# Optimization experiments

Measured on AMD Instinct MI355X. Metric: run time of the kernel, lower is better.

## Reference

```python
import jax, jax.numpy as jnp
import numpy as np

# Static hypernetwork layer sizes from HyperOption(z_dim=256, inner_h=64, a_dim=32, layers=3)
SIZES = [256 * 64, 64, 64 * 64, 64, 64 * 32, 32]  # sum = 22688
SPLITS = np.cumsum(SIZES)[:-1]


def setup_inputs() -> dict:
    key = jax.random.key(0)
    ks = jax.random.split(key, 8)
    B, Z, H = 4096, 256, 1024
    return {
        "inputs": jax.random.normal(ks[0], (B, Z), dtype=jnp.float32),
        "option": jax.random.normal(ks[1], (B, sum(SIZES)), dtype=jnp.float32) * 0.05,
        "w1": jax.random.normal(ks[2], (H, Z), dtype=jnp.float32) * 0.05,
        "b1": jax.random.normal(ks[3], (H,), dtype=jnp.float32) * 0.05,
        "w2": jax.random.normal(ks[4], (H, H), dtype=jnp.float32) * 0.05,
        "b2": jax.random.normal(ks[5], (H,), dtype=jnp.float32) * 0.05,
        "w3": jax.random.normal(ks[6], (1, H), dtype=jnp.float32) * 0.05,
        "b3": jax.random.normal(ks[7], (1,), dtype=jnp.float32) * 0.05,
    }


def _apply_option(state, option):
    # Per-sample hypernetwork MLP: weights/biases packed in `option`.
    parts = jnp.split(option, SPLITS, axis=-1)
    cur = state
    n_layers = len(parts) // 2
    for i in range(n_layers):
        w = parts[2 * i].reshape(option.shape[0], -1, cur.shape[-1])  # [B, out, in]
        b = parts[2 * i + 1]                                          # [B, out]
        cur = jnp.einsum('boi,bi->bo', w, cur) + b
        if i < n_layers - 1:
            cur = jax.nn.relu(cur)
    return cur


def _value(z, w1, b1, w2, b2, w3, b3):
    t = jax.nn.elu(z @ w1.T + b1)
    t = jax.nn.elu(t @ w2.T + b2)
    return t @ w3.T + b3  # [B, 1]


def reference(inputs, option, w1, b1, w2, b2, w3, b3):
    value = _value(inputs, w1, b1, w2, b2, w3, b3)   # [B, 1]
    action = _apply_option(inputs, option)            # [B, 32]
    return jnp.concatenate([value, action], axis=-1)  # [B, 33]
```

## Files before the change

kernel.cpp:

```cpp
#include <hip/hip_runtime.h>
#include <hip/hip_bf16.h>
#include <cstdint>

typedef __attribute__((ext_vector_type(8))) short  short8;
typedef __attribute__((ext_vector_type(8))) __bf16 bf16x8;
typedef __attribute__((ext_vector_type(4))) float  floatx4;
typedef __attribute__((ext_vector_type(4))) float  f32x4;
typedef __attribute__((ext_vector_type(4))) short  short4v;

union Frag { short8 s; bf16x8 b; };

__device__ inline short f2bf(float f) {
    union { float f; unsigned u; } v; v.f = f;
    unsigned r = (v.u + 0x7fffu + ((v.u >> 16) & 1u)) >> 16;
    return (short)r;
}
__device__ inline float elu(float x) { return x > 0.f ? x : __expf(x) - 1.f; }

__device__ inline short8 load8_f32_to_bf16(const float* __restrict__ p) {
    float4 f0 = ((const float4*)p)[0];
    float4 f1 = ((const float4*)p)[1];
    short8 r;
    r[0] = f2bf(f0.x); r[1] = f2bf(f0.y); r[2] = f2bf(f0.z); r[3] = f2bf(f0.w);
    r[4] = f2bf(f1.x); r[5] = f2bf(f1.y); r[6] = f2bf(f1.z); r[7] = f2bf(f1.w);
    return r;
}
__device__ inline float dot4(f32x4 a, f32x4 b) {
    return a.x * b.x + a.y * b.y + a.z * b.z + a.w * b.w;
}
__device__ inline f32x4 ntload4(const f32x4* __restrict__ p) {
    return __builtin_nontemporal_load(p);
}
__device__ inline float ntload1(const float* __restrict__ p) {
    return __builtin_nontemporal_load(p);
}

#define B_SZ   4096
#define Z_DIM  256
#define H_DIM  1024
#define OUT_W  33
#define OFF_W1 0
#define OFF_B1 16384
#define OFF_W2 16448
#define OFF_B2 20544
#define OFF_W3 20608
#define OFF_B3 22656
#define OPT_W  22688

#define G_BLOCKS 256
#define CONV_BLOCKS 64

template<int KTOT, int SM, int SN, bool ACONV, bool BCONV, bool VEPI>
__device__ __forceinline__ void gemm_tile(
    const void* __restrict__ Av, const void* __restrict__ Bv,
    const float* __restrict__ bias, const float* __restrict__ w3,
    __hip_bfloat16* __restrict__ T, float* __restrict__ out,
    int bm, int bn, int tid)
{
    const int lane = tid & 63, wid = tid >> 6;
    const int wm = wid >> 1, wn = wid & 1;
    const int m_wave = bm * (32 * SM) + wm * (16 * SM);
    const int n_wave = bn * (32 * SN) + wn * (16 * SN);
    const int lr = lane & 15, lk = (lane >> 4) * 8;

    floatx4 acc[SM][SN] = {};
    for (int k0 = 0; k0 < KTOT; k0 += 32) {
        Frag a[SM], bb[SN];
#pragma unroll
        for (int sm = 0; sm < SM; ++sm) {
            const size_t off = (size_t)(m_wave + sm * 16 + lr) * KTOT + k0 + lk;
            if constexpr (ACONV) a[sm].s = load8_f32_to_bf16((const float*)Av + off);
            else                 a[sm].s = *(const short8*)((const ushort*)Av + off);
        }
#pragma unroll
        for (int sn = 0; sn < SN; ++sn) {
            const size_t off = (size_t)(n_wave + sn * 16 + lr) * KTOT + k0 + lk;
            if constexpr (BCONV) bb[sn].s = load8_f32_to_bf16((const float*)Bv + off);
            else                 bb[sn].s = *(const short8*)((const ushort*)Bv + off);
        }
#pragma unroll
        for (int sm = 0; sm < SM; ++sm)
#pragma unroll
            for (int sn = 0; sn < SN; ++sn)
                acc[sm][sn] = __builtin_amdgcn_mfma_f32_16x16x32_bf16(
                    a[sm].b, bb[sn].b, acc[sm][sn], 0, 0, 0);
    }

    if constexpr (VEPI) {
        float bias_v[SN], w3_v[SN];
#pragma unroll
        for (int sn = 0; sn < SN; ++sn) {
            const int n = n_wave + sn * 16 + lr;
            bias_v[sn] = bias[n];
            w3_v[sn]   = w3[n];
        }
#pragma unroll
        for (int sm = 0; sm < SM; ++sm) {
#pragma unroll
            for (int r = 0; r < 4; ++r) {
                float rowsum = 0.f;
#pragma unroll
                for (int sn = 0; sn < SN; ++sn)
                    rowsum += elu(acc[sm][sn][r] + bias_v[sn]) * w3_v[sn];
                rowsum += __shfl_xor(rowsum, 1);
                rowsum += __shfl_xor(rowsum, 2);
                rowsum += __shfl_xor(rowsum, 4);
                rowsum += __shfl_xor(rowsum, 8);
                if (lr == 0) {
                    const int m = m_wave + sm * 16 + (lane >> 4) * 4 + r;
                    atomicAdd(out + (size_t)m * OUT_W, rowsum);
                }
            }
        }
    } else {
#pragma unroll
        for (int sm = 0; sm < SM; ++sm)
#pragma unroll
            for (int sn = 0; sn < SN; ++sn) {
                const int n = n_wave + sn * 16 + lr;
                const float bv = bias[n];
#pragma unroll
                for (int r = 0; r < 4; ++r) {
                    const int m = m_wave + sm * 16 + (lane >> 4) * 4 + r;
                    T[(size_t)m * H_DIM + n] = __float2bfloat16(elu(acc[sm][sn][r] + bv));
                }
            }
    }
}

__device__ __forceinline__ void hyper_l1(
    const float* __restrict__ z, const float* __restrict__ opt,
    float* __restrict__ h1ws, int b, int tid)
{
    const int lane = tid & 63, w = tid >> 6;
    const int l16 = lane & 15, lg = lane >> 4;
    const float* __restrict__ orow = opt + (size_t)b * OPT_W;

    const f32x4* __restrict__ Z4 = (const f32x4*)(z + (size_t)b * Z_DIM);
    f32x4 zv[4];
#pragma unroll
    for (int p = 0; p < 4; ++p) zv[p] = Z4[p * 16 + l16];

    const f32x4* __restrict__ W = (const f32x4*)(orow + OFF_W1) + (size_t)(w * 16) * 64;
    f32x4 wv[16];
#pragma unroll
    for (int g = 0; g < 4; ++g)
#pragma unroll
        for (int p = 0; p < 4; ++p)
            wv[g * 4 + p] = ntload4(W + (g * 4 + lg) * 64 + p * 16 + l16);

#pragma unroll
    for (int g = 0; g < 4; ++g) {
        float acc = 0.f;
#pragma unroll
        for (int p = 0; p < 4; ++p) acc += dot4(wv[g * 4 + p], zv[p]);
        acc += __shfl_xor(acc, 1);
        acc += __shfl_xor(acc, 2);
        acc += __shfl_xor(acc, 4);
        acc += __shfl_xor(acc, 8);
        const int r = 16 * w + g * 4 + lg;
        if (l16 == 0)
            h1ws[(size_t)b * 64 + r] = fmaxf(acc + ntload1(orow + OFF_B1 + r), 0.f);
    }
}

__device__ __forceinline__ void hyper_l23(
    const float* __restrict__ opt, const float* __restrict__ h1ws,
    float* __restrict__ out, int b, int tid, float* __restrict__ h2)
{
    const int lane = tid & 63, w = tid >> 6;
    const int l16 = lane & 15, lg = lane >> 4;
    const float* __restrict__ orow = opt + (size_t)b * OPT_W;

    const f32x4* __restrict__ W2 = (const f32x4*)(orow + OFF_W2) + (size_t)(w * 16) * 16;
    f32x4 wv2[4];
#pragma unroll
    for (int j = 0; j < 4; ++j) wv2[j] = ntload4(W2 + j * 64 + lane);

    const f32x4* __restrict__ W3 = (const f32x4*)(orow + OFF_W3) + (size_t)(w * 8) * 16;
    f32x4 wv3[2];
#pragma unroll
    for (int j = 0; j < 2; ++j) wv3[j] = ntload4(W3 + j * 64 + lane);

    const f32x4 h1v = *(const f32x4*)(h1ws + (size_t)b * 64 + 4 * l16);

#pragma unroll
    for (int j = 0; j < 4; ++j) {
        float p = dot4(wv2[j], h1v);
        p += __shfl_xor(p, 1); p += __shfl_xor(p, 2);
        p += __shfl_xor(p, 4); p += __shfl_xor(p, 8);
        const int r = 16 * w + j * 4 + lg;
        if (l16 == 0) h2[r] = fmaxf(p + ntload1(orow + OFF_B2 + r), 0.f);
    }
    __syncthreads();

    const f32x4 h2v = *(const f32x4*)(h2 + 4 * l16);
#pragma unroll
    for (int j = 0; j < 2; ++j) {
        float p = dot4(wv3[j], h2v);
        p += __shfl_xor(p, 1); p += __shfl_xor(p, 2);
        p += __shfl_xor(p, 4); p += __shfl_xor(p, 8);
        const int r = 8 * w + j * 4 + lg;
        if (l16 == 0) out[(size_t)b * OUT_W + 1 + r] = p + ntload1(orow + OFF_B3 + r);
    }
}

__global__ __launch_bounds__(256) void h1_kernel(
    const float* __restrict__ z, const float* __restrict__ opt,
    const float* __restrict__ w1, const float* __restrict__ b1,
    const float* __restrict__ w2, const float* __restrict__ b3,
    __hip_bfloat16* __restrict__ T1, __hip_bfloat16* __restrict__ w2bf,
    float* __restrict__ h1ws, float* __restrict__ out)
{
    const int blk = blockIdx.x, t = threadIdx.x;
    if (blk < G_BLOCKS) {
        const int j = (blk & 7) * 32 + (blk >> 3);
        gemm_tile<Z_DIM, 4, 4, true, true, false>(z, w1, b1, nullptr, T1, nullptr,
                                                  j >> 3, j & 7, t);
    } else if (blk < G_BLOCKS + CONV_BLOCKS) {
        const int gtid = (blk - G_BLOCKS) * 256 + t;
        if (gtid < B_SZ) out[(size_t)gtid * OUT_W] = b3[0];
#pragma unroll
        for (int i = 0; i < 16; ++i) {
            const int v = gtid + i * 16384;
            float4 f = ((const float4*)w2)[v];
            short4v s;
            s[0] = f2bf(f.x); s[1] = f2bf(f.y); s[2] = f2bf(f.z); s[3] = f2bf(f.w);
            ((short4v*)w2bf)[v] = s;
        }
    } else {
        hyper_l1(z, opt, h1ws, blk - (G_BLOCKS + CONV_BLOCKS), t);
    }
}

__global__ __launch_bounds__(256) void h23_kernel(
    const float* __restrict__ opt, const float* __restrict__ h1ws,
    const __hip_bfloat16* __restrict__ T1, const __hip_bfloat16* __restrict__ w2bf,
    const float* __restrict__ b2, const float* __restrict__ w3,
    float* __restrict__ out)
{
    __shared__ float h2[64];
    const int blk = blockIdx.x, t = threadIdx.x;
    if (blk < G_BLOCKS) {
        const int j = (blk & 7) * 32 + (blk >> 3);
        gemm_tile<H_DIM, 4, 4, false, false, true>(T1, w2bf, b2, w3, nullptr, out,
                                                   j >> 3, j & 7, t);
    } else {
        hyper_l23(opt, h1ws, out, blk - G_BLOCKS, t, h2);
    }
}

extern "C" void kernel_launch(void* const* d_in, const int* in_sizes, int n_in,
                              void* d_out, int out_size, void* d_ws, size_t ws_size,
                              hipStream_t stream)
{
    const float* z   = (const float*)d_in[0];
    const float* opt = (const float*)d_in[1];
    const float* w1  = (const float*)d_in[2];
    const float* b1  = (const float*)d_in[3];
    const float* w2  = (const float*)d_in[4];
    const float* b2  = (const float*)d_in[5];
    const float* w3  = (const float*)d_in[6];
    const float* b3  = (const float*)d_in[7];
    float* out = (float*)d_out;

    __hip_bfloat16* T1   = (__hip_bfloat16*)d_ws;
    __hip_bfloat16* w2bf = (__hip_bfloat16*)((char*)d_ws + 8u * 1024 * 1024);
    float*          h1ws = (float*)((char*)d_ws + 10u * 1024 * 1024);

    h1_kernel<<<dim3(G_BLOCKS + CONV_BLOCKS + B_SZ), dim3(256), 0, stream>>>(
        z, opt, w1, b1, w2, b3, T1, w2bf, h1ws, out);

    h23_kernel<<<dim3(G_BLOCKS + B_SZ), dim3(256), 0, stream>>>(
        opt, h1ws, T1, w2bf, b2, w3, out);
}
```

Baseline: 117.7 us.

## Split hypernetwork into three passes with row-per-wave mapping across blocks

```diff
diff --git a/kernel.cpp b/kernel.cpp
--- a/kernel.cpp
+++ b/kernel.cpp
@@ -33,6 +33,12 @@
 }
 __device__ inline float ntload1(const float* __restrict__ p) {
     return __builtin_nontemporal_load(p);
+}
+__device__ inline f32x4 relu4(f32x4 v) {
+    f32x4 r;
+    r.x = fmaxf(v.x, 0.f); r.y = fmaxf(v.y, 0.f);
+    r.z = fmaxf(v.z, 0.f); r.w = fmaxf(v.w, 0.f);
+    return r;
 }
 
 #define B_SZ   4096
@@ -49,6 +55,9 @@
 
 #define G_BLOCKS 256
 #define CONV_BLOCKS 64
+#define NB_H1 2048
+#define NB_H2 1024
+#define NB_H3 1024
 
 template<int KTOT, int SM, int SN, bool ACONV, bool BCONV, bool VEPI>
 __device__ __forceinline__ void gemm_tile(
@@ -128,84 +137,79 @@
     }
 }
 
-__device__ __forceinline__ void hyper_l1(
+__device__ __forceinline__ void h1_pass(
     const float* __restrict__ z, const float* __restrict__ opt,
-    float* __restrict__ h1ws, int b, int tid)
-{
-    const int lane = tid & 63, w = tid >> 6;
+    float* __restrict__ h1ws, int hb, int tid)
+{
+    const int wid = tid >> 6, lane = tid & 63;
+#pragma unroll
+    for (int t = 0; t < 16; ++t) {
+        const int Rb = t * 16384 + hb * 8 + wid * 2;
+        const int b0 = (Rb) >> 6,     r0 = (Rb) & 63;
+        const int b1i = (Rb + 1) >> 6, r1 = (Rb + 1) & 63;
+        f32x4 wv0 = ntload4((const f32x4*)(opt + (size_t)b0 * OPT_W + r0 * 256) + lane);
+        f32x4 wv1 = ntload4((const f32x4*)(opt + (size_t)b1i * OPT_W + r1 * 256) + lane);
+        f32x4 zv0 = *((const f32x4*)(z + (size_t)b0 * Z_DIM) + lane);
+        f32x4 zv1 = *((const f32x4*)(z + (size_t)b1i * Z_DIM) + lane);
+
+        float p0 = dot4(wv0, zv0);
+        float p1 = dot4(wv1, zv1);
+        p0 += __shfl_xor(p0, 1);  p1 += __shfl_xor(p1, 1);
+        p0 += __shfl_xor(p0, 2);  p1 += __shfl_xor(p1, 2);
+        p0 += __shfl_xor(p0, 4);  p1 += __shfl_xor(p1, 4);
+        p0 += __shfl_xor(p0, 8);  p1 += __shfl_xor(p1, 8);
+        p0 += __shfl_xor(p0, 16); p1 += __shfl_xor(p1, 16);
+        p0 += __shfl_xor(p0, 32); p1 += __shfl_xor(p1, 32);
+        if (lane == 0) {
+            h1ws[Rb]     = p0 + ntload1(opt + (size_t)b0 * OPT_W + OFF_B1 + r0);
+            h1ws[Rb + 1] = p1 + ntload1(opt + (size_t)b1i * OPT_W + OFF_B1 + r1);
+        }
+    }
+}
+
+__device__ __forceinline__ void h2_pass(
+    const float* __restrict__ opt, const float* __restrict__ h1ws,
+    float* __restrict__ h2ws, int hb, int tid)
+{
+    const int wid = tid >> 6, lane = tid & 63;
     const int l16 = lane & 15, lg = lane >> 4;
-    const float* __restrict__ orow = opt + (size_t)b * OPT_W;
-
-    const f32x4* __restrict__ Z4 = (const f32x4*)(z + (size_t)b * Z_DIM);
-    f32x4 zv[4];
-#pragma unroll
-    for (int p = 0; p < 4; ++p) zv[p] = Z4[p * 16 + l16];
-
-    const f32x4* __restrict__ W = (const f32x4*)(orow + OFF_W1) + (size_t)(w * 16) * 64;
-    f32x4 wv[16];
-#pragma unroll
-    for (int g = 0; g < 4; ++g)
-#pragma unroll
-        for (int p = 0; p < 4; ++p)
-            wv[g * 4 + p] = ntload4(W + (g * 4 + lg) * 64 + p * 16 + l16);
-
-#pragma unroll
-    for (int g = 0; g < 4; ++g) {
-        float acc = 0.f;
-#pragma unroll
-        for (int p = 0; p < 4; ++p) acc += dot4(wv[g * 4 + p], zv[p]);
-        acc += __shfl_xor(acc, 1);
-        acc += __shfl_xor(acc, 2);
-        acc += __shfl_xor(acc, 4);
-        acc += __shfl_xor(acc, 8);
-        const int r = 16 * w + g * 4 + lg;
-        if (l16 == 0)
-            h1ws[(size_t)b * 64 + r] = fmaxf(acc + ntload1(orow + OFF_B1 + r), 0.f);
-    }
-}
-
-__device__ __forceinline__ void hyper_l23(
-    const float* __restrict__ opt, const float* __restrict__ h1ws,
-    float* __restrict__ out, int b, int tid, float* __restrict__ h2)
-{
-    const int lane = tid & 63, w = tid >> 6;
-    const int l16 = lane & 15, lg = lane >> 4;
-    const float* __restrict__ orow = opt + (size_t)b * OPT_W;
-
-    const f32x4* __restrict__ W2 = (const f32x4*)(orow + OFF_W2) + (size_t)(w * 16) * 16;
-    f32x4 wv2[4];
-#pragma unroll
-    for (int j = 0; j < 4; ++j) wv2[j] = ntload4(W2 + j * 64 + lane);
-
-    const f32x4* __restrict__ W3 = (const f32x4*)(orow + OFF_W3) + (size_t)(w * 8) * 16;
-    f32x4 wv3[2];
-#pragma unroll
-    for (int j = 0; j < 2; ++j) wv3[j] = ntload4(W3 + j * 64 + lane);
-
-    const f32x4 h1v = *(const f32x4*)(h1ws + (size_t)b * 64 + 4 * l16);
-
-#pragma unroll
-    for (int j = 0; j < 4; ++j) {
-        float p = dot4(wv2[j], h1v);
+#pragma unroll
+    for (int t = 0; t < 16; ++t) {
+        const int R4 = t * 4096 + hb * 4 + wid;
+        const int b = R4 >> 4, q = R4 & 15;
+        f32x4 wv = ntload4((const f32x4*)(opt + (size_t)b * OPT_W + OFF_W2 + q * 256) + lane);
+        f32x4 hv = relu4(*(const f32x4*)(h1ws + (size_t)b * 64 + 4 * l16));
+        float p = dot4(wv, hv);
         p += __shfl_xor(p, 1); p += __shfl_xor(p, 2);
         p += __shfl_xor(p, 4); p += __shfl_xor(p, 8);
-        const int r = 16 * w + j * 4 + lg;
-        if (l16 == 0) h2[r] = fmaxf(p + ntload1(orow + OFF_B2 + r), 0.f);
-    }
-    __syncthreads();
-
-    const f32x4 h2v = *(const f32x4*)(h2 + 4 * l16);
-#pragma unroll
-    for (int j = 0; j < 2; ++j) {
-        float p = dot4(wv3[j], h2v);
+        const int r = 4 * q + lg;
+        if (l16 == 0)
+            h2ws[(size_t)b * 64 + r] = p + ntload1(opt + (size_t)b * OPT_W + OFF_B2 + r);
+    }
+}
+
+__device__ __forceinline__ void h3_pass(
+    const float* __restrict__ opt, const float* __restrict__ h2ws,
+    float* __restrict__ out, int hb, int tid)
+{
+    const int wid = tid >> 6, lane = tid & 63;
+    const int l16 = lane & 15, lg = lane >> 4;
+#pragma unroll
+    for (int t = 0; t < 8; ++t) {
+        const int R4 = t * 4096 + hb * 4 + wid;
+        const int b = R4 >> 3, q = R4 & 7;
+        f32x4 wv = ntload4((const f32x4*)(opt + (size_t)b * OPT_W + OFF_W3 + q * 256) + lane);
+        f32x4 hv = relu4(*(const f32x4*)(h2ws + (size_t)b * 64 + 4 * l16));
+        float p = dot4(wv, hv);
         p += __shfl_xor(p, 1); p += __shfl_xor(p, 2);
         p += __shfl_xor(p, 4); p += __shfl_xor(p, 8);
-        const int r = 8 * w + j * 4 + lg;
-        if (l16 == 0) out[(size_t)b * OUT_W + 1 + r] = p + ntload1(orow + OFF_B3 + r);
-    }
-}
-
-__global__ __launch_bounds__(256) void h1_kernel(
+        const int r = 4 * q + lg;
+        if (l16 == 0)
+            out[(size_t)b * OUT_W + 1 + r] = p + ntload1(opt + (size_t)b * OPT_W + OFF_B3 + r);
+    }
+}
+
+__global__ __launch_bounds__(256) void k1_kernel(
     const float* __restrict__ z, const float* __restrict__ opt,
     const float* __restrict__ w1, const float* __restrict__ b1,
     const float* __restrict__ w2, const float* __restrict__ b3,
@@ -229,25 +233,31 @@
             ((short4v*)w2bf)[v] = s;
         }
     } else {
-        hyper_l1(z, opt, h1ws, blk - (G_BLOCKS + CONV_BLOCKS), t);
-    }
-}
-
-__global__ __launch_bounds__(256) void h23_kernel(
+        h1_pass(z, opt, h1ws, blk - (G_BLOCKS + CONV_BLOCKS), t);
+    }
+}
+
+__global__ __launch_bounds__(256) void k2_kernel(
     const float* __restrict__ opt, const float* __restrict__ h1ws,
     const __hip_bfloat16* __restrict__ T1, const __hip_bfloat16* __restrict__ w2bf,
     const float* __restrict__ b2, const float* __restrict__ w3,
-    float* __restrict__ out)
-{
-    __shared__ float h2[64];
+    float* __restrict__ h2ws, float* __restrict__ out)
+{
     const int blk = blockIdx.x, t = threadIdx.x;
     if (blk < G_BLOCKS) {
         const int j = (blk & 7) * 32 + (blk >> 3);
         gemm_tile<H_DIM, 4, 4, false, false, true>(T1, w2bf, b2, w3, nullptr, out,
                                                    j >> 3, j & 7, t);
     } else {
-        hyper_l23(opt, h1ws, out, blk - G_BLOCKS, t, h2);
-    }
+        h2_pass(opt, h1ws, h2ws, blk - G_BLOCKS, t);
+    }
+}
+
+__global__ __launch_bounds__(256) void k3_kernel(
+    const float* __restrict__ opt, const float* __restrict__ h2ws,
+    float* __restrict__ out)
+{
+    h3_pass(opt, h2ws, out, blockIdx.x, threadIdx.x);
 }
 
 extern "C" void kernel_launch(void* const* d_in, const int* in_sizes, int n_in,
@@ -265,12 +275,15 @@
     float* out = (float*)d_out;
 
     __hip_bfloat16* T1   = (__hip_bfloat16*)d_ws;
-    __hip_bfloat16* w2bf = (__hip_bfloat16*)((char*)d_ws + 8u * 1024 * 1024);
-    float*          h1ws = (float*)((char*)d_ws + 10u * 1024 * 1024);
-
-    h1_kernel<<<dim3(G_BLOCKS + CONV_BLOCKS + B_SZ), dim3(256), 0, stream>>>(
+    __hip_bfloat16* w2bf = (__hip_bfloat16*)((char*)d_ws + 8u*1024*1024);
+    float*          h1ws = (float*)((char*)d_ws + 10u*1024*1024);
+    float*          h2ws = (float*)((char*)d_ws + 11u*1024*1024);
+
+    k1_kernel<<<dim3(G_BLOCKS + CONV_BLOCKS + NB_H1), dim3(256), 0, stream>>>(
         z, opt, w1, b1, w2, b3, T1, w2bf, h1ws, out);
 
-    h23_kernel<<<dim3(G_BLOCKS + B_SZ), dim3(256), 0, stream>>>(
-        opt, h1ws, T1, w2bf, b2, w3, out);
-}
+    k2_kernel<<<dim3(G_BLOCKS + NB_H2), dim3(256), 0, stream>>>(
+        opt, h1ws, T1, w2bf, b2, w3, h2ws, out);
+
+    k3_kernel<<<dim3(NB_H3), dim3(256), 0, stream>>>(opt, h2ws, out);
+}
```

Measured after the change: 179.6 us. +52.6%, slower.

## Fuse hypernetwork layers into persistent LDS-pipelined blocks split across both kernels

Applied to the files above, without the earlier changes.

```diff
diff --git a/kernel.cpp b/kernel.cpp
--- a/kernel.cpp
+++ b/kernel.cpp
@@ -28,27 +28,182 @@
 __device__ inline float dot4(f32x4 a, f32x4 b) {
     return a.x * b.x + a.y * b.y + a.z * b.z + a.w * b.w;
 }
-__device__ inline f32x4 ntload4(const f32x4* __restrict__ p) {
-    return __builtin_nontemporal_load(p);
-}
-__device__ inline float ntload1(const float* __restrict__ p) {
-    return __builtin_nontemporal_load(p);
+__device__ inline f32x4 relu4(f32x4 v) {
+    f32x4 r;
+    r.x = fmaxf(v.x, 0.f); r.y = fmaxf(v.y, 0.f);
+    r.z = fmaxf(v.z, 0.f); r.w = fmaxf(v.w, 0.f);
+    return r;
 }
 
 #define B_SZ   4096
 #define Z_DIM  256
 #define H_DIM  1024
 #define OUT_W  33
-#define OFF_W1 0
-#define OFF_B1 16384
-#define OFF_W2 16448
-#define OFF_B2 20544
-#define OFF_W3 20608
-#define OFF_B3 22656
 #define OPT_W  22688
 
 #define G_BLOCKS 256
 #define CONV_BLOCKS 64
+#define HYP_BLOCKS 256
+#define SPB 8
+
+#define LQ0   0
+#define LQSZ  16384
+#define LC    49152
+#define LZ    77824
+#define LH1   78848
+#define LH2   79104
+#define LDS_TOTAL 79360
+
+__device__ __forceinline__ void gload16(const void* g, void* l) {
+    __builtin_amdgcn_global_load_lds((const uint32_t*)g, (uint32_t*)l, 16, 0, 0);
+}
+#define WAITVM(N) do { asm volatile("s_waitcnt vmcnt(" #N ") lgkmcnt(0)" ::: "memory"); \
+                       __builtin_amdgcn_sched_barrier(0); } while (0)
+#define WAITLGKM() do { asm volatile("s_waitcnt lgkmcnt(0)" ::: "memory"); \
+                        __builtin_amdgcn_sched_barrier(0); } while (0)
+#define SBAR() __builtin_amdgcn_s_barrier()
+
+__device__ __forceinline__ void stage_q(const float* __restrict__ orow, int q,
+                                        char* smem, int buf, int w, int lane) {
+    const float* gbase = orow + q * 4096;
+    char* lbase = smem + LQ0 + buf * LQSZ;
+#pragma unroll
+    for (int i = 0; i < 4; ++i) {
+        const int c = i * 4 + w;
+        gload16(gbase + c * 256 + lane * 4, lbase + c * 1024);
+    }
+}
+__device__ __forceinline__ void stage_z(const float* __restrict__ z, int smp,
+                                        char* smem, int lane) {
+    gload16(z + (size_t)smp * Z_DIM + lane * 4, smem + LZ);
+}
+__device__ __forceinline__ void stage_c(const float* __restrict__ orow,
+                                        const float* __restrict__ optBase,
+                                        const float* __restrict__ gLast,
+                                        char* smem, int w, int lane) {
+    const float* gbase = orow + 16384;
+#pragma unroll
+    for (int i = 0; i < 7; ++i) {
+        const int c = i * 4 + w;
+        const float* gp = gbase + c * 256 + lane * 4;
+        gp = (gp > gLast) ? optBase : gp;
+        gload16(gp, smem + LC + c * 1024);
+    }
+}
+
+__device__ __forceinline__ void hyper_block(
+    const float* __restrict__ z, const float* __restrict__ opt,
+    float* __restrict__ out, int baseSample, int tid, char* smem)
+{
+    const int w = tid >> 6, lane = tid & 63;
+    const int l16 = lane & 15, lg = lane >> 4;
+    const float* gLast = opt + (size_t)B_SZ * OPT_W - 4;
+    float* h1raw = (float*)(smem + LH1);
+    float* h2raw = (float*)(smem + LH2);
+
+    {
+        const float* orow0 = opt + (size_t)baseSample * OPT_W;
+        stage_q(orow0, 0, smem, 0, w, lane);
+        stage_z(z, baseSample, smem, lane);
+        stage_q(orow0, 1, smem, 1, w, lane);
+        stage_q(orow0, 2, smem, 2, w, lane);
+    }
+
+    for (int s = 0; s < SPB; ++s) {
+        const int smp = baseSample + s;
+        const int snx = baseSample + ((s + 1) & (SPB - 1));
+        const float* orow  = opt + (size_t)smp * OPT_W;
+        const float* orowN = opt + (size_t)snx * OPT_W;
+        const int m = s % 3;
+
+        WAITVM(8); SBAR();
+        stage_c(orow, opt, gLast, smem, w, lane);
+        f32x4 zv[4];
+#pragma unroll
+        for (int p = 0; p < 4; ++p)
+            zv[p] = *(const f32x4*)(smem + LZ + (p * 16 + l16) * 16);
+        {
+            const char* Qb = smem + LQ0 + m * LQSZ;
+            float acc = 0.f;
+#pragma unroll
+            for (int p = 0; p < 4; ++p)
+                acc += dot4(*(const f32x4*)(Qb + (w * 4 + lg) * 1024 + (p * 16 + l16) * 16), zv[p]);
+            acc += __shfl_xor(acc, 1); acc += __shfl_xor(acc, 2);
+            acc += __shfl_xor(acc, 4); acc += __shfl_xor(acc, 8);
+            if (l16 == 0) h1raw[w * 4 + lg] = acc;
+        }
+        WAITVM(11); SBAR();
+        stage_q(orow, 3, smem, m, w, lane);
+        {
+            const char* Qb = smem + LQ0 + ((m + 1) % 3) * LQSZ;
+            float acc = 0.f;
+#pragma unroll
+            for (int p = 0; p < 4; ++p)
+                acc += dot4(*(const f32x4*)(Qb + (w * 4 + lg) * 1024 + (p * 16 + l16) * 16), zv[p]);
+            acc += __shfl_xor(acc, 1); acc += __shfl_xor(acc, 2);
+            acc += __shfl_xor(acc, 4); acc += __shfl_xor(acc, 8);
+            if (l16 == 0) h1raw[16 + w * 4 + lg] = acc;
+        }
+        WAITVM(11); SBAR();
+        stage_q(orowN, 0, smem, (m + 1) % 3, w, lane);
+        stage_z(z, snx, smem, lane);
+        {
+            const char* Qb = smem + LQ0 + ((m + 2) % 3) * LQSZ;
+            float acc = 0.f;
+#pragma unroll
+            for (int p = 0; p < 4; ++p)
+                acc += dot4(*(const f32x4*)(Qb + (w * 4 + lg) * 1024 + (p * 16 + l16) * 16), zv[p]);
+            acc += __shfl_xor(acc, 1); acc += __shfl_xor(acc, 2);
+            acc += __shfl_xor(acc, 4); acc += __shfl_xor(acc, 8);
+            if (l16 == 0) h1raw[32 + w * 4 + lg] = acc;
+        }
+        WAITVM(5); SBAR();
+        stage_q(orowN, 1, smem, (m + 2) % 3, w, lane);
+        {
+            const char* Qb = smem + LQ0 + m * LQSZ;
+            float acc = 0.f;
+#pragma unroll
+            for (int p = 0; p < 4; ++p)
+                acc += dot4(*(const f32x4*)(Qb + (w * 4 + lg) * 1024 + (p * 16 + l16) * 16), zv[p]);
+            acc += __shfl_xor(acc, 1); acc += __shfl_xor(acc, 2);
+            acc += __shfl_xor(acc, 4); acc += __shfl_xor(acc, 8);
+            if (l16 == 0) h1raw[48 + w * 4 + lg] = acc;
+        }
+        WAITVM(9); SBAR();
+        stage_q(orowN, 2, smem, m, w, lane);
+        const float* C = (const float*)(smem + LC);
+        {
+            f32x4 h1v = *(const f32x4*)(h1raw + 4 * l16);
+            f32x4 b1v = *(const f32x4*)(C + 4 * l16);
+            h1v = relu4(h1v + b1v);
+#pragma unroll
+            for (int j = 0; j < 4; ++j) {
+                const int r = 16 * w + j * 4 + lg;
+                f32x4 wv = *(const f32x4*)(C + 64 + r * 64 + 4 * l16);
+                float p = dot4(wv, h1v);
+                p += __shfl_xor(p, 1); p += __shfl_xor(p, 2);
+                p += __shfl_xor(p, 4); p += __shfl_xor(p, 8);
+                if (l16 == 0) h2raw[r] = p;
+            }
+        }
+        WAITLGKM(); SBAR();
+        {
+            f32x4 h2v = *(const f32x4*)(h2raw + 4 * l16);
+            f32x4 b2v = *(const f32x4*)(C + 4160 + 4 * l16);
+            h2v = relu4(h2v + b2v);
+#pragma unroll
+            for (int j = 0; j < 2; ++j) {
+                const int r = 8 * w + j * 4 + lg;
+                f32x4 wv = *(const f32x4*)(C + 4224 + r * 64 + 4 * l16);
+                float p = dot4(wv, h2v);
+                p += __shfl_xor(p, 1); p += __shfl_xor(p, 2);
+                p += __shfl_xor(p, 4); p += __shfl_xor(p, 8);
+                if (l16 == 0)
+                    out[(size_t)smp * OUT_W + 1 + r] = p + C[6272 + r];
+            }
+        }
+    }
+}
 
 template<int KTOT, int SM, int SN, bool ACONV, bool BCONV, bool VEPI>
 __device__ __forceinline__ void gemm_tile(
@@ -107,8 +262,8 @@
                 rowsum += __shfl_xor(rowsum, 4);
                 rowsum += __shfl_xor(rowsum, 8);
                 if (lr == 0) {
-                    const int m = m_wave + sm * 16 + (lane >> 4) * 4 + r;
-                    atomicAdd(out + (size_t)m * OUT_W, rowsum);
+                    const int mm = m_wave + sm * 16 + (lane >> 4) * 4 + r;
+                    atomicAdd(out + (size_t)mm * OUT_W, rowsum);
                 }
             }
         }
@@ -121,132 +276,58 @@
                 const float bv = bias[n];
 #pragma unroll
                 for (int r = 0; r < 4; ++r) {
-                    const int m = m_wave + sm * 16 + (lane >> 4) * 4 + r;
-                    T[(size_t)m * H_DIM + n] = __float2bfloat16(elu(acc[sm][sn][r] + bv));
+                    const int mm = m_wave + sm * 16 + (lane >> 4) * 4 + r;
+                    T[(size_t)mm * H_DIM + n] = __float2bfloat16(elu(acc[sm][sn][r] + bv));
                 }
             }
     }
 }
 
-__device__ __forceinline__ void hyper_l1(
-    const float* __restrict__ z, const float* __restrict__ opt,
-    float* __restrict__ h1ws, int b, int tid)
-{
-    const int lane = tid & 63, w = tid >> 6;
-    const int l16 = lane & 15, lg = lane >> 4;
-    const float* __restrict__ orow = opt + (size_t)b * OPT_W;
-
-    const f32x4* __restrict__ Z4 = (const f32x4*)(z + (size_t)b * Z_DIM);
-    f32x4 zv[4];
-#pragma unroll
-    for (int p = 0; p < 4; ++p) zv[p] = Z4[p * 16 + l16];
-
-    const f32x4* __restrict__ W = (const f32x4*)(orow + OFF_W1) + (size_t)(w * 16) * 64;
-    f32x4 wv[16];
-#pragma unroll
-    for (int g = 0; g < 4; ++g)
-#pragma unroll
-        for (int p = 0; p < 4; ++p)
-            wv[g * 4 + p] = ntload4(W + (g * 4 + lg) * 64 + p * 16 + l16);
-
-#pragma unroll
-    for (int g = 0; g < 4; ++g) {
-        float acc = 0.f;
-#pragma unroll
-        for (int p = 0; p < 4; ++p) acc += dot4(wv[g * 4 + p], zv[p]);
-        acc += __shfl_xor(acc, 1);
-        acc += __shfl_xor(acc, 2);
-        acc += __shfl_xor(acc, 4);
-        acc += __shfl_xor(acc, 8);
-        const int r = 16 * w + g * 4 + lg;
-        if (l16 == 0)
-            h1ws[(size_t)b * 64 + r] = fmaxf(acc + ntload1(orow + OFF_B1 + r), 0.f);
-    }
-}
-
-__device__ __forceinline__ void hyper_l23(
-    const float* __restrict__ opt, const float* __restrict__ h1ws,
-    float* __restrict__ out, int b, int tid, float* __restrict__ h2)
-{
-    const int lane = tid & 63, w = tid >> 6;
-    const int l16 = lane & 15, lg = lane >> 4;
-    const float* __restrict__ orow = opt + (size_t)b * OPT_W;
-
-    const f32x4* __restrict__ W2 = (const f32x4*)(orow + OFF_W2) + (size_t)(w * 16) * 16;
-    f32x4 wv2[4];
-#pragma unroll
-    for (int j = 0; j < 4; ++j) wv2[j] = ntload4(W2 + j * 64 + lane);
-
-    const f32x4* __restrict__ W3 = (const f32x4*)(orow + OFF_W3) + (size_t)(w * 8) * 16;
-    f32x4 wv3[2];
-#pragma unroll
-    for (int j = 0; j < 2; ++j) wv3[j] = ntload4(W3 + j * 64 + lane);
-
-    const f32x4 h1v = *(const f32x4*)(h1ws + (size_t)b * 64 + 4 * l16);
-
-#pragma unroll
-    for (int j = 0; j < 4; ++j) {
-        float p = dot4(wv2[j], h1v);
-        p += __shfl_xor(p, 1); p += __shfl_xor(p, 2);
-        p += __shfl_xor(p, 4); p += __shfl_xor(p, 8);
-        const int r = 16 * w + j * 4 + lg;
-        if (l16 == 0) h2[r] = fmaxf(p + ntload1(orow + OFF_B2 + r), 0.f);
-    }
-    __syncthreads();
-
-    const f32x4 h2v = *(const f32x4*)(h2 + 4 * l16);
-#pragma unroll
-    for (int j = 0; j < 2; ++j) {
-        float p = dot4(wv3[j], h2v);
-        p += __shfl_xor(p, 1); p += __shfl_xor(p, 2);
-        p += __shfl_xor(p, 4); p += __shfl_xor(p, 8);
-        const int r = 8 * w + j * 4 + lg;
-        if (l16 == 0) out[(size_t)b * OUT_W + 1 + r] = p + ntload1(orow + OFF_B3 + r);
-    }
-}
-
-__global__ __launch_bounds__(256) void h1_kernel(
+__global__ __launch_bounds__(256) void k1_kernel(
     const float* __restrict__ z, const float* __restrict__ opt,
     const float* __restrict__ w1, const float* __restrict__ b1,
     const float* __restrict__ w2, const float* __restrict__ b3,
     __hip_bfloat16* __restrict__ T1, __hip_bfloat16* __restrict__ w2bf,
-    float* __restrict__ h1ws, float* __restrict__ out)
-{
+    float* __restrict__ out)
+{
+    __shared__ __align__(16) char smem[LDS_TOTAL];
     const int blk = blockIdx.x, t = threadIdx.x;
-    if (blk < G_BLOCKS) {
-        const int j = (blk & 7) * 32 + (blk >> 3);
+    if (blk < HYP_BLOCKS) {
+        hyper_block(z, opt, out, blk * SPB, t, smem);
+    } else if (blk < HYP_BLOCKS + G_BLOCKS) {
+        const int j0 = blk - HYP_BLOCKS;
+        const int j = (j0 & 7) * 32 + (j0 >> 3);
         gemm_tile<Z_DIM, 4, 4, true, true, false>(z, w1, b1, nullptr, T1, nullptr,
                                                   j >> 3, j & 7, t);
-    } else if (blk < G_BLOCKS + CONV_BLOCKS) {
-        const int gtid = (blk - G_BLOCKS) * 256 + t;
+    } else {
+        const int gtid = (blk - HYP_BLOCKS - G_BLOCKS) * 256 + t;
         if (gtid < B_SZ) out[(size_t)gtid * OUT_W] = b3[0];
 #pragma unroll
         for (int i = 0; i < 16; ++i) {
             const int v = gtid + i * 16384;
             float4 f = ((const float4*)w2)[v];
-            short4v s;
-            s[0] = f2bf(f.x); s[1] = f2bf(f.y); s[2] = f2bf(f.z); s[3] = f2bf(f.w);
-            ((short4v*)w2bf)[v] = s;
-        }
-    } else {
-        hyper_l1(z, opt, h1ws, blk - (G_BLOCKS + CONV_BLOCKS), t);
-    }
-}
-
-__global__ __launch_bounds__(256) void h23_kernel(
-    const float* __restrict__ opt, const float* __restrict__ h1ws,
+            short4v sv;
+            sv[0] = f2bf(f.x); sv[1] = f2bf(f.y); sv[2] = f2bf(f.z); sv[3] = f2bf(f.w);
+            ((short4v*)w2bf)[v] = sv;
+        }
+    }
+}
+
+__global__ __launch_bounds__(256) void k2_kernel(
+    const float* __restrict__ z, const float* __restrict__ opt,
     const __hip_bfloat16* __restrict__ T1, const __hip_bfloat16* __restrict__ w2bf,
     const float* __restrict__ b2, const float* __restrict__ w3,
     float* __restrict__ out)
 {
-    __shared__ float h2[64];
+    __shared__ __align__(16) char smem[LDS_TOTAL];
     const int blk = blockIdx.x, t = threadIdx.x;
-    if (blk < G_BLOCKS) {
-        const int j = (blk & 7) * 32 + (blk >> 3);
+    if (blk < HYP_BLOCKS) {
+        hyper_block(z, opt, out, 2048 + blk * SPB, t, smem);
+    } else {
+        const int j0 = blk - HYP_BLOCKS;
+        const int j = (j0 & 7) * 32 + (j0 >> 3);
         gemm_tile<H_DIM, 4, 4, false, false, true>(T1, w2bf, b2, w3, nullptr, out,
                                                    j >> 3, j & 7, t);
-    } else {
-        hyper_l23(opt, h1ws, out, blk - G_BLOCKS, t, h2);
     }
 }
 
@@ -266,11 +347,10 @@
 
     __hip_bfloat16* T1   = (__hip_bfloat16*)d_ws;
     __hip_bfloat16* w2bf = (__hip_bfloat16*)((char*)d_ws + 8u * 1024 * 1024);
-    float*          h1ws = (float*)((char*)d_ws + 10u * 1024 * 1024);
-
-    h1_kernel<<<dim3(G_BLOCKS + CONV_BLOCKS + B_SZ), dim3(256), 0, stream>>>(
-        z, opt, w1, b1, w2, b3, T1, w2bf, h1ws, out);
-
-    h23_kernel<<<dim3(G_BLOCKS + B_SZ), dim3(256), 0, stream>>>(
-        opt, h1ws, T1, w2bf, b2, w3, out);
-}
+
+    k1_kernel<<<dim3(HYP_BLOCKS + G_BLOCKS + CONV_BLOCKS), dim3(256), 0, stream>>>(
+        z, opt, w1, b1, w2, b3, T1, w2bf, out);
+
+    k2_kernel<<<dim3(HYP_BLOCKS + G_BLOCKS), dim3(256), 0, stream>>>(
+        z, opt, T1, w2bf, b2, w3, out);
+}
```

Measured after the change: 111.1 us. 5.6% less time.
